# Performance work log

Hardware: AMD Instinct MI355X
Metric: run time of the kernel (lower is better)

Reference implementation:

```python
import jax, jax.numpy as jnp
import numpy as np


def setup_inputs() -> dict:
    key = jax.random.key(0)
    k1, k2 = jax.random.split(key)
    E, D, N = 1600000, 32, 100000
    e = jax.random.normal(k1, (E, D), dtype=jnp.float32)
    dst = jax.random.randint(k2, (E,), 0, N, dtype=jnp.int64)
    return {"e": e, "dst": dst, "n_nodes": N}


def reference(e, dst, n_nodes):
    # copy_e + mean reducer == segment mean of edge features over dst nodes.
    # DGL yields 0 for nodes with no in-edges.
    sums = jax.ops.segment_sum(e, dst, num_segments=n_nodes)          # [N, D]
    counts = jax.ops.segment_sum(jnp.ones((e.shape[0],), e.dtype), dst,
                                 num_segments=n_nodes)                 # [N]
    denom = jnp.maximum(counts, 1.0)[:, None]
    return sums / denom
```

## Files before the change

kernel.cpp:

```cpp
#include <hip/hip_runtime.h>
#include <hip/hip_bf16.h>


#define D_FEAT 32
#define NPB 64
#define NB_MAX 2048
#define STAGE_MAX 8192
#define CAP_MAX 2048
#define CURSOR_PAD 16

__global__ __launch_bounds__(256) void bucket_bin_kernel(
    const int* __restrict__ dst,
    int* __restrict__ cursor,
    unsigned int* __restrict__ buckets,
    int E, int nb, int cap, int chunk)
{
    __shared__ int hist[NB_MAX];
    __shared__ int offs[NB_MAX];
    __shared__ int run [NB_MAX];
    __shared__ int gpos[NB_MAX];
    __shared__ unsigned int   st_rec[STAGE_MAX];
    __shared__ unsigned short st_b  [STAGE_MAX];
    __shared__ int scan_s[256];

    int t = threadIdx.x;
    int cstart = blockIdx.x * chunk;
    int cn = E - cstart; if (cn > chunk) cn = chunk;
    if (cn <= 0) return;

    for (int i = t; i < nb; i += 256) hist[i] = 0;
    __syncthreads();

    for (int i = t; i < cn; i += 256) {
        int d = dst[cstart + i];
        atomicAdd(&hist[d >> 6], 1);
    }
    __syncthreads();

    int q = (nb + 255) / 256;
    int lo = t * q, hi = lo + q; if (hi > nb) hi = nb;
    int sum = 0;
    for (int i = lo; i < hi; i++) sum += hist[i];
    scan_s[t] = sum;
    __syncthreads();
    for (int off = 1; off < 256; off <<= 1) {
        int v = (t >= off) ? scan_s[t - off] : 0;
        __syncthreads();
        scan_s[t] += v;
        __syncthreads();
    }
    int ex = scan_s[t] - sum;
    for (int i = lo; i < hi; i++) {
        offs[i] = ex;
        run[i]  = ex;
        ex += hist[i];
    }
    __syncthreads();

    for (int i = t; i < nb; i += 256) {
        int h = hist[i];
        gpos[i] = (h > 0) ? atomicAdd(&cursor[i * CURSOR_PAD], h) : 0;
    }

    for (int i = t; i < cn; i += 256) {
        int g = cstart + i;
        int d = dst[g];
        int b = d >> 6;
        int p = atomicAdd(&run[b], 1);
        st_rec[p] = ((unsigned)g << 6) | (unsigned)(d & 63);
        st_b[p]   = (unsigned short)b;
    }
    __syncthreads();

    for (int p = t; p < cn; p += 256) {
        int b = st_b[p];
        int rel = gpos[b] + (p - offs[b]);
        if (rel < cap)
            buckets[(size_t)b * cap + rel] = st_rec[p];
    }
}

__global__ __launch_bounds__(256) void node_sort_kernel(
    const unsigned int* __restrict__ buckets,
    const int* __restrict__ cursor,
    unsigned int* __restrict__ ids2,
    int* __restrict__ startArr,
    int* __restrict__ cntArr,
    int N, int cap)
{
    __shared__ int hist[NPB];
    __shared__ int sc  [NPB];
    __shared__ int run [NPB];
    __shared__ unsigned int st[CAP_MAX];
    int t = threadIdx.x;
    int b = blockIdx.x;

    if (t < NPB) hist[t] = 0;
    __syncthreads();

    int m = cursor[b * CURSOR_PAD]; if (m > cap) m = cap;
    const unsigned int* rec = buckets + (size_t)b * cap;

    for (int i = t; i < m; i += 256)
        atomicAdd(&hist[rec[i] & 63], 1);
    __syncthreads();

    if (t < NPB) sc[t] = hist[t];
    __syncthreads();
    for (int off = 1; off < NPB; off <<= 1) {
        int v = 0;
        if (t < NPB && t >= off) v = sc[t - off];
        __syncthreads();
        if (t < NPB) sc[t] += v;
        __syncthreads();
    }
    if (t < NPB) { sc[t] -= hist[t]; run[t] = sc[t]; }
    __syncthreads();

    for (int i = t; i < m; i += 256) {
        unsigned r = rec[i];
        int p = atomicAdd(&run[r & 63], 1);
        st[p] = r >> 6;
    }
    __syncthreads();

    for (int i = t; i < m; i += 256)
        ids2[(size_t)b * cap + i] = st[i];
    if (t < NPB) {
        int node = b * NPB + t;
        if (node < N) {
            startArr[node] = b * cap + sc[t];
            cntArr[node]   = hist[t];
        }
    }
}

__global__ __launch_bounds__(256) void gather_kernel(
    const float4* __restrict__ e4,
    const unsigned int* __restrict__ ids,
    const int* __restrict__ startArr,
    const int* __restrict__ cntArr,
    float4* __restrict__ out4,
    int N, int fixed_stride)
{
    int node = blockIdx.x * 32 + (threadIdx.x >> 3);
    int j = threadIdx.x & 7;
    if (node >= N) return;
    int c = cntArr[node];
    int s;
    if (fixed_stride > 0) {
        s = node * fixed_stride;
        if (c > fixed_stride) c = fixed_stride;
    } else {
        s = startArr[node];
    }
    float4 a0 = {0.f,0.f,0.f,0.f}, a1 = {0.f,0.f,0.f,0.f};
    float4 a2 = {0.f,0.f,0.f,0.f}, a3 = {0.f,0.f,0.f,0.f};
    int k = 0;
    for (; k + 4 <= c; k += 4) {
        unsigned e0 = ids[s+k], e1 = ids[s+k+1], e2 = ids[s+k+2], e3 = ids[s+k+3];
        float4 v0 = e4[(size_t)e0*8 + j];
        float4 v1 = e4[(size_t)e1*8 + j];
        float4 v2 = e4[(size_t)e2*8 + j];
        float4 v3 = e4[(size_t)e3*8 + j];
        a0.x += v0.x; a0.y += v0.y; a0.z += v0.z; a0.w += v0.w;
        a1.x += v1.x; a1.y += v1.y; a1.z += v1.z; a1.w += v1.w;
        a2.x += v2.x; a2.y += v2.y; a2.z += v2.z; a2.w += v2.w;
        a3.x += v3.x; a3.y += v3.y; a3.z += v3.z; a3.w += v3.w;
    }
    for (; k < c; k++) {
        unsigned e0 = ids[s+k];
        float4 v0 = e4[(size_t)e0*8 + j];
        a0.x += v0.x; a0.y += v0.y; a0.z += v0.z; a0.w += v0.w;
    }
    float inv = 1.0f / (float)(c > 1 ? c : 1);
    float4 r;
    r.x = (a0.x + a1.x + a2.x + a3.x) * inv;
    r.y = (a0.y + a1.y + a2.y + a3.y) * inv;
    r.z = (a0.z + a1.z + a2.z + a3.z) * inv;
    r.w = (a0.w + a1.w + a2.w + a3.w) * inv;
    out4[(size_t)node * 8 + j] = r;
}

#define SLOT_STRIDE 64
__global__ __launch_bounds__(256) void scatter_ids_fixed(
    const int* __restrict__ dst, int* __restrict__ cursor,
    unsigned int* __restrict__ ids, int E)
{
    int i = blockIdx.x * 256 + threadIdx.x;
    if (i >= E) return;
    int d = dst[i];
    int pos = atomicAdd(&cursor[d], 1);
    if (pos < SLOT_STRIDE) ids[d * SLOT_STRIDE + pos] = (unsigned)i;
}

__global__ __launch_bounds__(256) void scatter_atomic_kernel(
    const float4* __restrict__ e4, const int* __restrict__ dst,
    float* __restrict__ sums, int* __restrict__ counts, int total)
{
    int t = blockIdx.x * 256 + threadIdx.x;
    if (t >= total) return;
    int edge = t >> 3;
    int fq = t & 7;
    float4 v = e4[t];
    int d = dst[edge];
    float* o = sums + (size_t)d * D_FEAT + fq * 4;
    atomicAdd(o + 0, v.x);
    atomicAdd(o + 1, v.y);
    atomicAdd(o + 2, v.z);
    atomicAdd(o + 3, v.w);
    if (fq == 0) atomicAdd(counts + d, 1);
}

__global__ __launch_bounds__(256) void finalize_kernel(
    float4* __restrict__ out4, const int* __restrict__ counts, int total)
{
    int t = blockIdx.x * 256 + threadIdx.x;
    if (t >= total) return;
    int node = t >> 3;
    int c = counts[node];
    float inv = 1.0f / (float)(c > 1 ? c : 1);
    float4 v = out4[t];
    v.x *= inv; v.y *= inv; v.z *= inv; v.w *= inv;
    out4[t] = v;
}

extern "C" void kernel_launch(void* const* d_in, const int* in_sizes, int n_in,
                              void* d_out, int out_size, void* d_ws, size_t ws_size,
                              hipStream_t stream) {
    const float4* e4 = (const float4*)d_in[0];
    const int* dst = (const int*)d_in[1];
    int E = in_sizes[0] / D_FEAT;
    int N = out_size / D_FEAT;

    int nb = (N + NPB - 1) / NPB;
    long long avg = (E + nb - 1) / nb;
    long long thresh = avg + 8 * (long long)(__builtin_sqrt((double)avg)) + 64;
    int cap = (int)((thresh + 63) / 64 * 64);

    char* ws = (char*)d_ws;
    size_t fast_need = (size_t)nb * CURSOR_PAD * 4
                     + (size_t)nb * cap * 4 * 2
                     + (size_t)N * 4 * 2;
    size_t r2_need = (size_t)N * 4 + (size_t)N * SLOT_STRIDE * 4;

    if (nb <= NB_MAX && cap <= CAP_MAX && ws_size >= fast_need) {
        int* cursor = (int*)ws;
        unsigned int* buckets = (unsigned int*)(ws + (size_t)nb * CURSOR_PAD * 4);
        unsigned int* ids2 = buckets + (size_t)nb * cap;
        int* startArr = (int*)(ids2 + (size_t)nb * cap);
        int* cntArr = startArr + N;

        hipMemsetAsync(cursor, 0, (size_t)nb * CURSOR_PAD * 4, stream);

        int grid1 = 256;
        int chunk = (E + grid1 - 1) / grid1;
        if (chunk > STAGE_MAX) { grid1 = (E + STAGE_MAX - 1) / STAGE_MAX; chunk = STAGE_MAX; }
        bucket_bin_kernel<<<grid1, 256, 0, stream>>>(dst, cursor, buckets, E, nb, cap, chunk);
        node_sort_kernel<<<nb, 256, 0, stream>>>(buckets, cursor, ids2, startArr, cntArr, N, cap);
        gather_kernel<<<(N + 31) / 32, 256, 0, stream>>>(e4, ids2, startArr, cntArr,
                                                         (float4*)d_out, N, 0);
    } else if (ws_size >= r2_need) {
        int* cursor = (int*)ws;
        unsigned int* ids = (unsigned int*)(ws + (size_t)N * 4);
        hipMemsetAsync(cursor, 0, (size_t)N * 4, stream);
        scatter_ids_fixed<<<(E + 255) / 256, 256, 0, stream>>>(dst, cursor, ids, E);
        gather_kernel<<<(N + 31) / 32, 256, 0, stream>>>(e4, ids, nullptr, cursor,
                                                         (float4*)d_out, N, SLOT_STRIDE);
    } else {
        int* counts = (int*)ws;
        hipMemsetAsync(d_out, 0, (size_t)out_size * sizeof(float), stream);
        hipMemsetAsync(counts, 0, (size_t)N * 4, stream);
        int total = E * (D_FEAT / 4);
        scatter_atomic_kernel<<<(total + 255) / 256, 256, 0, stream>>>(
            e4, dst, (float*)d_out, counts, total);
        int fin = N * (D_FEAT / 4);
        finalize_kernel<<<(fin + 255) / 256, 256, 0, stream>>>(
            (float4*)d_out, counts, fin);
    }
}
```

Before: 348.6 us.

## Replace two-level bucket sort with global histogram, scan and atomic scatter CSR build

Result: slower. 500.3 us (+43.5%).

```diff
diff --git a/kernel.cpp b/kernel.cpp
--- a/kernel.cpp
+++ b/kernel.cpp
@@ -1,137 +1,122 @@
 #include <hip/hip_runtime.h>
-#include <hip/hip_bf16.h>
 
 
 #define D_FEAT 32
-#define NPB 64
-#define NB_MAX 2048
-#define STAGE_MAX 8192
-#define CAP_MAX 2048
-#define CURSOR_PAD 16
-
-__global__ __launch_bounds__(256) void bucket_bin_kernel(
-    const int* __restrict__ dst,
-    int* __restrict__ cursor,
-    unsigned int* __restrict__ buckets,
-    int E, int nb, int cap, int chunk)
-{
-    __shared__ int hist[NB_MAX];
-    __shared__ int offs[NB_MAX];
-    __shared__ int run [NB_MAX];
-    __shared__ int gpos[NB_MAX];
-    __shared__ unsigned int   st_rec[STAGE_MAX];
-    __shared__ unsigned short st_b  [STAGE_MAX];
-    __shared__ int scan_s[256];
-
+#define SCAN_SPAN 1024
+
+__global__ __launch_bounds__(256) void hist_kernel(
+    const int* __restrict__ dst, int* __restrict__ cnt, int E)
+{
+    int base = (blockIdx.x * 256 + threadIdx.x) * 4;
+    if (base + 3 < E) {
+        int4 d = *(const int4*)(dst + base);
+        atomicAdd(&cnt[d.x], 1);
+        atomicAdd(&cnt[d.y], 1);
+        atomicAdd(&cnt[d.z], 1);
+        atomicAdd(&cnt[d.w], 1);
+    } else {
+        for (int i = base; i < E; i++) atomicAdd(&cnt[dst[i]], 1);
+    }
+}
+
+__global__ __launch_bounds__(256) void scan_block_sums(
+    const int* __restrict__ cnt, int* __restrict__ bsum, int N)
+{
+    __shared__ int red[256];
     int t = threadIdx.x;
-    int cstart = blockIdx.x * chunk;
-    int cn = E - cstart; if (cn > chunk) cn = chunk;
-    if (cn <= 0) return;
-
-    for (int i = t; i < nb; i += 256) hist[i] = 0;
+    int base = blockIdx.x * SCAN_SPAN + t * 4;
+    int s = 0;
+    if (base + 3 < N) {
+        int4 v = *(const int4*)(cnt + base);
+        s = v.x + v.y + v.z + v.w;
+    } else {
+        for (int i = base; i < N; i++) s += cnt[i];
+    }
+    red[t] = s;
     __syncthreads();
-
-    for (int i = t; i < cn; i += 256) {
-        int d = dst[cstart + i];
-        atomicAdd(&hist[d >> 6], 1);
-    }
-    __syncthreads();
-
-    int q = (nb + 255) / 256;
-    int lo = t * q, hi = lo + q; if (hi > nb) hi = nb;
-    int sum = 0;
-    for (int i = lo; i < hi; i++) sum += hist[i];
-    scan_s[t] = sum;
+    for (int off = 128; off > 0; off >>= 1) {
+        if (t < off) red[t] += red[t + off];
+        __syncthreads();
+    }
+    if (t == 0) bsum[blockIdx.x] = red[0];
+}
+
+__global__ __launch_bounds__(256) void scan_bases(
+    const int* __restrict__ bsum, int* __restrict__ bbase, int nblk)
+{
+    __shared__ int sc[256];
+    int t = threadIdx.x;
+    int v = (t < nblk) ? bsum[t] : 0;
+    int orig = v;
+    sc[t] = v;
     __syncthreads();
     for (int off = 1; off < 256; off <<= 1) {
-        int v = (t >= off) ? scan_s[t - off] : 0;
-        __syncthreads();
-        scan_s[t] += v;
-        __syncthreads();
-    }
-    int ex = scan_s[t] - sum;
-    for (int i = lo; i < hi; i++) {
-        offs[i] = ex;
-        run[i]  = ex;
-        ex += hist[i];
-    }
+        int u = (t >= off) ? sc[t - off] : 0;
+        __syncthreads();
+        sc[t] += u;
+        __syncthreads();
+    }
+    if (t < nblk) bbase[t] = sc[t] - orig;
+}
+
+__global__ __launch_bounds__(256) void scan_write(
+    const int* __restrict__ cnt, const int* __restrict__ bbase,
+    int* __restrict__ startArr, int* __restrict__ run, int N)
+{
+    __shared__ int sc[256];
+    int t = threadIdx.x;
+    int base = blockIdx.x * SCAN_SPAN + t * 4;
+    int c0 = 0, c1 = 0, c2 = 0, c3 = 0;
+    if (base + 3 < N) {
+        int4 v = *(const int4*)(cnt + base);
+        c0 = v.x; c1 = v.y; c2 = v.z; c3 = v.w;
+    } else {
+        if (base     < N) c0 = cnt[base];
+        if (base + 1 < N) c1 = cnt[base + 1];
+        if (base + 2 < N) c2 = cnt[base + 2];
+        if (base + 3 < N) c3 = cnt[base + 3];
+    }
+    int s = c0 + c1 + c2 + c3;
+    int orig = s;
+    sc[t] = s;
     __syncthreads();
-
-    for (int i = t; i < nb; i += 256) {
-        int h = hist[i];
-        gpos[i] = (h > 0) ? atomicAdd(&cursor[i * CURSOR_PAD], h) : 0;
-    }
-
-    for (int i = t; i < cn; i += 256) {
-        int g = cstart + i;
-        int d = dst[g];
-        int b = d >> 6;
-        int p = atomicAdd(&run[b], 1);
-        st_rec[p] = ((unsigned)g << 6) | (unsigned)(d & 63);
-        st_b[p]   = (unsigned short)b;
-    }
-    __syncthreads();
-
-    for (int p = t; p < cn; p += 256) {
-        int b = st_b[p];
-        int rel = gpos[b] + (p - offs[b]);
-        if (rel < cap)
-            buckets[(size_t)b * cap + rel] = st_rec[p];
-    }
-}
-
-__global__ __launch_bounds__(256) void node_sort_kernel(
-    const unsigned int* __restrict__ buckets,
-    const int* __restrict__ cursor,
-    unsigned int* __restrict__ ids2,
-    int* __restrict__ startArr,
-    int* __restrict__ cntArr,
-    int N, int cap)
-{
-    __shared__ int hist[NPB];
-    __shared__ int sc  [NPB];
-    __shared__ int run [NPB];
-    __shared__ unsigned int st[CAP_MAX];
-    int t = threadIdx.x;
-    int b = blockIdx.x;
-
-    if (t < NPB) hist[t] = 0;
-    __syncthreads();
-
-    int m = cursor[b * CURSOR_PAD]; if (m > cap) m = cap;
-    const unsigned int* rec = buckets + (size_t)b * cap;
-
-    for (int i = t; i < m; i += 256)
-        atomicAdd(&hist[rec[i] & 63], 1);
-    __syncthreads();
-
-    if (t < NPB) sc[t] = hist[t];
-    __syncthreads();
-    for (int off = 1; off < NPB; off <<= 1) {
-        int v = 0;
-        if (t < NPB && t >= off) v = sc[t - off];
-        __syncthreads();
-        if (t < NPB) sc[t] += v;
-        __syncthreads();
-    }
-    if (t < NPB) { sc[t] -= hist[t]; run[t] = sc[t]; }
-    __syncthreads();
-
-    for (int i = t; i < m; i += 256) {
-        unsigned r = rec[i];
-        int p = atomicAdd(&run[r & 63], 1);
-        st[p] = r >> 6;
-    }
-    __syncthreads();
-
-    for (int i = t; i < m; i += 256)
-        ids2[(size_t)b * cap + i] = st[i];
-    if (t < NPB) {
-        int node = b * NPB + t;
-        if (node < N) {
-            startArr[node] = b * cap + sc[t];
-            cntArr[node]   = hist[t];
-        }
+    for (int off = 1; off < 256; off <<= 1) {
+        int u = (t >= off) ? sc[t - off] : 0;
+        __syncthreads();
+        sc[t] += u;
+        __syncthreads();
+    }
+    int ex = bbase[blockIdx.x] + sc[t] - orig;
+    int p0 = ex, p1 = ex + c0, p2 = p1 + c1, p3 = p2 + c2;
+    if (base + 3 < N) {
+        *(int4*)(startArr + base) = make_int4(p0, p1, p2, p3);
+        *(int4*)(run + base)      = make_int4(p0, p1, p2, p3);
+    } else {
+        if (base     < N) { startArr[base]     = p0; run[base]     = p0; }
+        if (base + 1 < N) { startArr[base + 1] = p1; run[base + 1] = p1; }
+        if (base + 2 < N) { startArr[base + 2] = p2; run[base + 2] = p2; }
+        if (base + 3 < N) { startArr[base + 3] = p3; run[base + 3] = p3; }
+    }
+}
+
+__global__ __launch_bounds__(256) void scatter_kernel(
+    const int* __restrict__ dst, int* __restrict__ run,
+    unsigned int* __restrict__ ids, int E)
+{
+    int base = (blockIdx.x * 256 + threadIdx.x) * 4;
+    if (base + 3 < E) {
+        int4 d = *(const int4*)(dst + base);
+        int p0 = atomicAdd(&run[d.x], 1);
+        int p1 = atomicAdd(&run[d.y], 1);
+        int p2 = atomicAdd(&run[d.z], 1);
+        int p3 = atomicAdd(&run[d.w], 1);
+        ids[p0] = (unsigned)base;
+        ids[p1] = (unsigned)base + 1;
+        ids[p2] = (unsigned)base + 2;
+        ids[p3] = (unsigned)base + 3;
+    } else {
+        for (int i = base; i < E; i++)
+            ids[atomicAdd(&run[dst[i]], 1)] = (unsigned)i;
     }
 }
 
@@ -141,22 +126,36 @@
     const int* __restrict__ startArr,
     const int* __restrict__ cntArr,
     float4* __restrict__ out4,
-    int N, int fixed_stride)
+    int N)
 {
     int node = blockIdx.x * 32 + (threadIdx.x >> 3);
     int j = threadIdx.x & 7;
     if (node >= N) return;
     int c = cntArr[node];
-    int s;
-    if (fixed_stride > 0) {
-        s = node * fixed_stride;
-        if (c > fixed_stride) c = fixed_stride;
-    } else {
-        s = startArr[node];
-    }
+    int s = startArr[node];
     float4 a0 = {0.f,0.f,0.f,0.f}, a1 = {0.f,0.f,0.f,0.f};
     float4 a2 = {0.f,0.f,0.f,0.f}, a3 = {0.f,0.f,0.f,0.f};
     int k = 0;
+    for (; k + 8 <= c; k += 8) {
+        unsigned e0 = ids[s+k],   e1 = ids[s+k+1], e2 = ids[s+k+2], e3 = ids[s+k+3];
+        unsigned e4i = ids[s+k+4], e5 = ids[s+k+5], e6 = ids[s+k+6], e7 = ids[s+k+7];
+        float4 v0 = e4[(size_t)e0*8  + j];
+        float4 v1 = e4[(size_t)e1*8  + j];
+        float4 v2 = e4[(size_t)e2*8  + j];
+        float4 v3 = e4[(size_t)e3*8  + j];
+        float4 v4 = e4[(size_t)e4i*8 + j];
+        float4 v5 = e4[(size_t)e5*8  + j];
+        float4 v6 = e4[(size_t)e6*8  + j];
+        float4 v7 = e4[(size_t)e7*8  + j];
+        a0.x += v0.x; a0.y += v0.y; a0.z += v0.z; a0.w += v0.w;
+        a1.x += v1.x; a1.y += v1.y; a1.z += v1.z; a1.w += v1.w;
+        a2.x += v2.x; a2.y += v2.y; a2.z += v2.z; a2.w += v2.w;
+        a3.x += v3.x; a3.y += v3.y; a3.z += v3.z; a3.w += v3.w;
+        a0.x += v4.x; a0.y += v4.y; a0.z += v4.z; a0.w += v4.w;
+        a1.x += v5.x; a1.y += v5.y; a1.z += v5.z; a1.w += v5.w;
+        a2.x += v6.x; a2.y += v6.y; a2.z += v6.z; a2.w += v6.w;
+        a3.x += v7.x; a3.y += v7.y; a3.z += v7.z; a3.w += v7.w;
+    }
     for (; k + 4 <= c; k += 4) {
         unsigned e0 = ids[s+k], e1 = ids[s+k+1], e2 = ids[s+k+2], e3 = ids[s+k+3];
         float4 v0 = e4[(size_t)e0*8 + j];
@@ -180,18 +179,6 @@
     r.z = (a0.z + a1.z + a2.z + a3.z) * inv;
     r.w = (a0.w + a1.w + a2.w + a3.w) * inv;
     out4[(size_t)node * 8 + j] = r;
-}
-
-#define SLOT_STRIDE 64
-__global__ __launch_bounds__(256) void scatter_ids_fixed(
-    const int* __restrict__ dst, int* __restrict__ cursor,
-    unsigned int* __restrict__ ids, int E)
-{
-    int i = blockIdx.x * 256 + threadIdx.x;
-    if (i >= E) return;
-    int d = dst[i];
-    int pos = atomicAdd(&cursor[d], 1);
-    if (pos < SLOT_STRIDE) ids[d * SLOT_STRIDE + pos] = (unsigned)i;
 }
 
 __global__ __launch_bounds__(256) void scatter_atomic_kernel(
@@ -233,40 +220,29 @@
     int E = in_sizes[0] / D_FEAT;
     int N = out_size / D_FEAT;
 
-    int nb = (N + NPB - 1) / NPB;
-    long long avg = (E + nb - 1) / nb;
-    long long thresh = avg + 8 * (long long)(__builtin_sqrt((double)avg)) + 64;
-    int cap = (int)((thresh + 63) / 64 * 64);
+    int nblk = (N + SCAN_SPAN - 1) / SCAN_SPAN;
 
     char* ws = (char*)d_ws;
-    size_t fast_need = (size_t)nb * CURSOR_PAD * 4
-                     + (size_t)nb * cap * 4 * 2
-                     + (size_t)N * 4 * 2;
-    size_t r2_need = (size_t)N * 4 + (size_t)N * SLOT_STRIDE * 4;
-
-    if (nb <= NB_MAX && cap <= CAP_MAX && ws_size >= fast_need) {
-        int* cursor = (int*)ws;
-        unsigned int* buckets = (unsigned int*)(ws + (size_t)nb * CURSOR_PAD * 4);
-        unsigned int* ids2 = buckets + (size_t)nb * cap;
-        int* startArr = (int*)(ids2 + (size_t)nb * cap);
-        int* cntArr = startArr + N;
-
-        hipMemsetAsync(cursor, 0, (size_t)nb * CURSOR_PAD * 4, stream);
-
-        int grid1 = 256;
-        int chunk = (E + grid1 - 1) / grid1;
-        if (chunk > STAGE_MAX) { grid1 = (E + STAGE_MAX - 1) / STAGE_MAX; chunk = STAGE_MAX; }
-        bucket_bin_kernel<<<grid1, 256, 0, stream>>>(dst, cursor, buckets, E, nb, cap, chunk);
-        node_sort_kernel<<<nb, 256, 0, stream>>>(buckets, cursor, ids2, startArr, cntArr, N, cap);
-        gather_kernel<<<(N + 31) / 32, 256, 0, stream>>>(e4, ids2, startArr, cntArr,
-                                                         (float4*)d_out, N, 0);
-    } else if (ws_size >= r2_need) {
-        int* cursor = (int*)ws;
-        unsigned int* ids = (unsigned int*)(ws + (size_t)N * 4);
-        hipMemsetAsync(cursor, 0, (size_t)N * 4, stream);
-        scatter_ids_fixed<<<(E + 255) / 256, 256, 0, stream>>>(dst, cursor, ids, E);
-        gather_kernel<<<(N + 31) / 32, 256, 0, stream>>>(e4, ids, nullptr, cursor,
-                                                         (float4*)d_out, N, SLOT_STRIDE);
+    size_t need = ((size_t)3 * N + 512) * 4 + (size_t)E * 4;
+
+    if (nblk <= 256 && ws_size >= need) {
+        int* cnt      = (int*)ws;
+        int* startArr = cnt + N;
+        int* run      = startArr + N;
+        int* bsum     = run + N;
+        int* bbase    = bsum + 256;
+        unsigned int* ids = (unsigned int*)(bbase + 256);
+
+        hipMemsetAsync(cnt, 0, (size_t)N * 4, stream);
+
+        int gE = (E + 1023) / 1024;
+        hist_kernel<<<gE, 256, 0, stream>>>(dst, cnt, E);
+        scan_block_sums<<<nblk, 256, 0, stream>>>(cnt, bsum, N);
+        scan_bases<<<1, 256, 0, stream>>>(bsum, bbase, nblk);
+        scan_write<<<nblk, 256, 0, stream>>>(cnt, bbase, startArr, run, N);
+        scatter_kernel<<<gE, 256, 0, stream>>>(dst, run, ids, E);
+        gather_kernel<<<(N + 31) / 32, 256, 0, stream>>>(e4, ids, startArr, cnt,
+                                                         (float4*)d_out, N);
     } else {
         int* counts = (int*)ws;
         hipMemsetAsync(d_out, 0, (size_t)out_size * sizeof(float), stream);
```

## Fuse node sort and gather into per-bucket LDS atomic accumulation kernel

Applied to the files above, without the earlier changes.

Result: slower. 539.1 us (+54.6%).

```diff
diff --git a/kernel.cpp b/kernel.cpp
--- a/kernel.cpp
+++ b/kernel.cpp
@@ -1,28 +1,20 @@
 #include <hip/hip_runtime.h>
-#include <hip/hip_bf16.h>
 
 
 #define D_FEAT 32
 #define NPB 64
 #define NB_MAX 2048
-#define STAGE_MAX 8192
-#define CAP_MAX 2048
 #define CURSOR_PAD 16
 
-__global__ __launch_bounds__(256) void bucket_bin_kernel(
+__global__ __launch_bounds__(256) void bin_kernel(
     const int* __restrict__ dst,
     int* __restrict__ cursor,
     unsigned int* __restrict__ buckets,
     int E, int nb, int cap, int chunk)
 {
     __shared__ int hist[NB_MAX];
-    __shared__ int offs[NB_MAX];
+    __shared__ int gpos[NB_MAX];
     __shared__ int run [NB_MAX];
-    __shared__ int gpos[NB_MAX];
-    __shared__ unsigned int   st_rec[STAGE_MAX];
-    __shared__ unsigned short st_b  [STAGE_MAX];
-    __shared__ int scan_s[256];
-
     int t = threadIdx.x;
     int cstart = blockIdx.x * chunk;
     int cn = E - cstart; if (cn > chunk) cn = chunk;
@@ -31,167 +23,114 @@
     for (int i = t; i < nb; i += 256) hist[i] = 0;
     __syncthreads();
 
-    for (int i = t; i < cn; i += 256) {
-        int d = dst[cstart + i];
-        atomicAdd(&hist[d >> 6], 1);
-    }
-    __syncthreads();
-
-    int q = (nb + 255) / 256;
-    int lo = t * q, hi = lo + q; if (hi > nb) hi = nb;
-    int sum = 0;
-    for (int i = lo; i < hi; i++) sum += hist[i];
-    scan_s[t] = sum;
-    __syncthreads();
-    for (int off = 1; off < 256; off <<= 1) {
-        int v = (t >= off) ? scan_s[t - off] : 0;
-        __syncthreads();
-        scan_s[t] += v;
-        __syncthreads();
-    }
-    int ex = scan_s[t] - sum;
-    for (int i = lo; i < hi; i++) {
-        offs[i] = ex;
-        run[i]  = ex;
-        ex += hist[i];
-    }
+    int nv = cn >> 2;
+    const int4* d4 = (const int4*)(dst + cstart);
+    for (int i = t; i < nv; i += 256) {
+        int4 d = d4[i];
+        atomicAdd(&hist[d.x >> 6], 1);
+        atomicAdd(&hist[d.y >> 6], 1);
+        atomicAdd(&hist[d.z >> 6], 1);
+        atomicAdd(&hist[d.w >> 6], 1);
+    }
+    for (int i = (nv << 2) + t; i < cn; i += 256)
+        atomicAdd(&hist[dst[cstart + i] >> 6], 1);
     __syncthreads();
 
     for (int i = t; i < nb; i += 256) {
         int h = hist[i];
         gpos[i] = (h > 0) ? atomicAdd(&cursor[i * CURSOR_PAD], h) : 0;
-    }
-
-    for (int i = t; i < cn; i += 256) {
+        run[i] = 0;
+    }
+    __syncthreads();
+
+    for (int i = t; i < nv; i += 256) {
+        int4 d = d4[i];
+        int g = cstart + (i << 2);
+        int b0 = d.x >> 6, b1 = d.y >> 6, b2 = d.z >> 6, b3 = d.w >> 6;
+        int p0 = gpos[b0] + atomicAdd(&run[b0], 1);
+        int p1 = gpos[b1] + atomicAdd(&run[b1], 1);
+        int p2 = gpos[b2] + atomicAdd(&run[b2], 1);
+        int p3 = gpos[b3] + atomicAdd(&run[b3], 1);
+        if (p0 < cap) buckets[(size_t)b0 * cap + p0] = ((unsigned)(g    ) << 6) | (unsigned)(d.x & 63);
+        if (p1 < cap) buckets[(size_t)b1 * cap + p1] = ((unsigned)(g + 1) << 6) | (unsigned)(d.y & 63);
+        if (p2 < cap) buckets[(size_t)b2 * cap + p2] = ((unsigned)(g + 2) << 6) | (unsigned)(d.z & 63);
+        if (p3 < cap) buckets[(size_t)b3 * cap + p3] = ((unsigned)(g + 3) << 6) | (unsigned)(d.w & 63);
+    }
+    for (int i = (nv << 2) + t; i < cn; i += 256) {
         int g = cstart + i;
         int d = dst[g];
         int b = d >> 6;
-        int p = atomicAdd(&run[b], 1);
-        st_rec[p] = ((unsigned)g << 6) | (unsigned)(d & 63);
-        st_b[p]   = (unsigned short)b;
-    }
-    __syncthreads();
-
-    for (int p = t; p < cn; p += 256) {
-        int b = st_b[p];
-        int rel = gpos[b] + (p - offs[b]);
-        if (rel < cap)
-            buckets[(size_t)b * cap + rel] = st_rec[p];
-    }
-}
-
-__global__ __launch_bounds__(256) void node_sort_kernel(
+        int p = gpos[b] + atomicAdd(&run[b], 1);
+        if (p < cap) buckets[(size_t)b * cap + p] = ((unsigned)g << 6) | (unsigned)(d & 63);
+    }
+}
+
+__global__ __launch_bounds__(256) void bucket_accum_kernel(
+    const float4* __restrict__ e4,
     const unsigned int* __restrict__ buckets,
     const int* __restrict__ cursor,
-    unsigned int* __restrict__ ids2,
-    int* __restrict__ startArr,
-    int* __restrict__ cntArr,
+    float4* __restrict__ out4,
     int N, int cap)
 {
-    __shared__ int hist[NPB];
-    __shared__ int sc  [NPB];
-    __shared__ int run [NPB];
-    __shared__ unsigned int st[CAP_MAX];
+    __shared__ float sums[NPB][33];
+    __shared__ int cnt[NPB];
     int t = threadIdx.x;
     int b = blockIdx.x;
 
-    if (t < NPB) hist[t] = 0;
+    for (int i = t; i < NPB * 33; i += 256) ((float*)sums)[i] = 0.f;
+    if (t < NPB) cnt[t] = 0;
     __syncthreads();
 
     int m = cursor[b * CURSOR_PAD]; if (m > cap) m = cap;
     const unsigned int* rec = buckets + (size_t)b * cap;
 
-    for (int i = t; i < m; i += 256)
-        atomicAdd(&hist[rec[i] & 63], 1);
-    __syncthreads();
-
-    if (t < NPB) sc[t] = hist[t];
-    __syncthreads();
-    for (int off = 1; off < NPB; off <<= 1) {
-        int v = 0;
-        if (t < NPB && t >= off) v = sc[t - off];
-        __syncthreads();
-        if (t < NPB) sc[t] += v;
-        __syncthreads();
-    }
-    if (t < NPB) { sc[t] -= hist[t]; run[t] = sc[t]; }
-    __syncthreads();
-
-    for (int i = t; i < m; i += 256) {
-        unsigned r = rec[i];
-        int p = atomicAdd(&run[r & 63], 1);
-        st[p] = r >> 6;
-    }
-    __syncthreads();
-
-    for (int i = t; i < m; i += 256)
-        ids2[(size_t)b * cap + i] = st[i];
-    if (t < NPB) {
-        int node = b * NPB + t;
+    int g = t >> 3, j = t & 7;
+    int jb = j * 4;
+    int i = g;
+    for (; i + 96 < m; i += 128) {
+        unsigned r0 = rec[i], r1 = rec[i + 32], r2 = rec[i + 64], r3 = rec[i + 96];
+        float4 v0 = e4[(size_t)(r0 >> 6) * 8 + j];
+        float4 v1 = e4[(size_t)(r1 >> 6) * 8 + j];
+        float4 v2 = e4[(size_t)(r2 >> 6) * 8 + j];
+        float4 v3 = e4[(size_t)(r3 >> 6) * 8 + j];
+        int l0 = r0 & 63, l1 = r1 & 63, l2 = r2 & 63, l3 = r3 & 63;
+        atomicAdd(&sums[l0][jb + 0], v0.x); atomicAdd(&sums[l0][jb + 1], v0.y);
+        atomicAdd(&sums[l0][jb + 2], v0.z); atomicAdd(&sums[l0][jb + 3], v0.w);
+        atomicAdd(&sums[l1][jb + 0], v1.x); atomicAdd(&sums[l1][jb + 1], v1.y);
+        atomicAdd(&sums[l1][jb + 2], v1.z); atomicAdd(&sums[l1][jb + 3], v1.w);
+        atomicAdd(&sums[l2][jb + 0], v2.x); atomicAdd(&sums[l2][jb + 1], v2.y);
+        atomicAdd(&sums[l2][jb + 2], v2.z); atomicAdd(&sums[l2][jb + 3], v2.w);
+        atomicAdd(&sums[l3][jb + 0], v3.x); atomicAdd(&sums[l3][jb + 1], v3.y);
+        atomicAdd(&sums[l3][jb + 2], v3.z); atomicAdd(&sums[l3][jb + 3], v3.w);
+        if (j == 0) {
+            atomicAdd(&cnt[l0], 1); atomicAdd(&cnt[l1], 1);
+            atomicAdd(&cnt[l2], 1); atomicAdd(&cnt[l3], 1);
+        }
+    }
+    for (; i < m; i += 32) {
+        unsigned r0 = rec[i];
+        float4 v0 = e4[(size_t)(r0 >> 6) * 8 + j];
+        int l0 = r0 & 63;
+        atomicAdd(&sums[l0][jb + 0], v0.x); atomicAdd(&sums[l0][jb + 1], v0.y);
+        atomicAdd(&sums[l0][jb + 2], v0.z); atomicAdd(&sums[l0][jb + 3], v0.w);
+        if (j == 0) atomicAdd(&cnt[l0], 1);
+    }
+    __syncthreads();
+
+    for (int s = t; s < NPB * 8; s += 256) {
+        int local = s >> 3, jj = (s & 7) * 4;
+        int node = b * NPB + local;
         if (node < N) {
-            startArr[node] = b * cap + sc[t];
-            cntArr[node]   = hist[t];
+            int c = cnt[local];
+            float inv = 1.0f / (float)(c > 1 ? c : 1);
+            float4 r;
+            r.x = sums[local][jj + 0] * inv;
+            r.y = sums[local][jj + 1] * inv;
+            r.z = sums[local][jj + 2] * inv;
+            r.w = sums[local][jj + 3] * inv;
+            out4[(size_t)node * 8 + (s & 7)] = r;
         }
     }
-}
-
-__global__ __launch_bounds__(256) void gather_kernel(
-    const float4* __restrict__ e4,
-    const unsigned int* __restrict__ ids,
-    const int* __restrict__ startArr,
-    const int* __restrict__ cntArr,
-    float4* __restrict__ out4,
-    int N, int fixed_stride)
-{
-    int node = blockIdx.x * 32 + (threadIdx.x >> 3);
-    int j = threadIdx.x & 7;
-    if (node >= N) return;
-    int c = cntArr[node];
-    int s;
-    if (fixed_stride > 0) {
-        s = node * fixed_stride;
-        if (c > fixed_stride) c = fixed_stride;
-    } else {
-        s = startArr[node];
-    }
-    float4 a0 = {0.f,0.f,0.f,0.f}, a1 = {0.f,0.f,0.f,0.f};
-    float4 a2 = {0.f,0.f,0.f,0.f}, a3 = {0.f,0.f,0.f,0.f};
-    int k = 0;
-    for (; k + 4 <= c; k += 4) {
-        unsigned e0 = ids[s+k], e1 = ids[s+k+1], e2 = ids[s+k+2], e3 = ids[s+k+3];
-        float4 v0 = e4[(size_t)e0*8 + j];
-        float4 v1 = e4[(size_t)e1*8 + j];
-        float4 v2 = e4[(size_t)e2*8 + j];
-        float4 v3 = e4[(size_t)e3*8 + j];
-        a0.x += v0.x; a0.y += v0.y; a0.z += v0.z; a0.w += v0.w;
-        a1.x += v1.x; a1.y += v1.y; a1.z += v1.z; a1.w += v1.w;
-        a2.x += v2.x; a2.y += v2.y; a2.z += v2.z; a2.w += v2.w;
-        a3.x += v3.x; a3.y += v3.y; a3.z += v3.z; a3.w += v3.w;
-    }
-    for (; k < c; k++) {
-        unsigned e0 = ids[s+k];
-        float4 v0 = e4[(size_t)e0*8 + j];
-        a0.x += v0.x; a0.y += v0.y; a0.z += v0.z; a0.w += v0.w;
-    }
-    float inv = 1.0f / (float)(c > 1 ? c : 1);
-    float4 r;
-    r.x = (a0.x + a1.x + a2.x + a3.x) * inv;
-    r.y = (a0.y + a1.y + a2.y + a3.y) * inv;
-    r.z = (a0.z + a1.z + a2.z + a3.z) * inv;
-    r.w = (a0.w + a1.w + a2.w + a3.w) * inv;
-    out4[(size_t)node * 8 + j] = r;
-}
-
-#define SLOT_STRIDE 64
-__global__ __launch_bounds__(256) void scatter_ids_fixed(
-    const int* __restrict__ dst, int* __restrict__ cursor,
-    unsigned int* __restrict__ ids, int E)
-{
-    int i = blockIdx.x * 256 + threadIdx.x;
-    if (i >= E) return;
-    int d = dst[i];
-    int pos = atomicAdd(&cursor[d], 1);
-    if (pos < SLOT_STRIDE) ids[d * SLOT_STRIDE + pos] = (unsigned)i;
 }
 
 __global__ __launch_bounds__(256) void scatter_atomic_kernel(
@@ -240,33 +179,20 @@
 
     char* ws = (char*)d_ws;
     size_t fast_need = (size_t)nb * CURSOR_PAD * 4
-                     + (size_t)nb * cap * 4 * 2
-                     + (size_t)N * 4 * 2;
-    size_t r2_need = (size_t)N * 4 + (size_t)N * SLOT_STRIDE * 4;
-
-    if (nb <= NB_MAX && cap <= CAP_MAX && ws_size >= fast_need) {
+                     + (size_t)nb * cap * 4;
+
+    if (nb <= NB_MAX && E <= (1 << 26) && ws_size >= fast_need) {
         int* cursor = (int*)ws;
         unsigned int* buckets = (unsigned int*)(ws + (size_t)nb * CURSOR_PAD * 4);
-        unsigned int* ids2 = buckets + (size_t)nb * cap;
-        int* startArr = (int*)(ids2 + (size_t)nb * cap);
-        int* cntArr = startArr + N;
 
         hipMemsetAsync(cursor, 0, (size_t)nb * CURSOR_PAD * 4, stream);
 
-        int grid1 = 256;
-        int chunk = (E + grid1 - 1) / grid1;
-        if (chunk > STAGE_MAX) { grid1 = (E + STAGE_MAX - 1) / STAGE_MAX; chunk = STAGE_MAX; }
-        bucket_bin_kernel<<<grid1, 256, 0, stream>>>(dst, cursor, buckets, E, nb, cap, chunk);
-        node_sort_kernel<<<nb, 256, 0, stream>>>(buckets, cursor, ids2, startArr, cntArr, N, cap);
-        gather_kernel<<<(N + 31) / 32, 256, 0, stream>>>(e4, ids2, startArr, cntArr,
-                                                         (float4*)d_out, N, 0);
-    } else if (ws_size >= r2_need) {
-        int* cursor = (int*)ws;
-        unsigned int* ids = (unsigned int*)(ws + (size_t)N * 4);
-        hipMemsetAsync(cursor, 0, (size_t)N * 4, stream);
-        scatter_ids_fixed<<<(E + 255) / 256, 256, 0, stream>>>(dst, cursor, ids, E);
-        gather_kernel<<<(N + 31) / 32, 256, 0, stream>>>(e4, ids, nullptr, cursor,
-                                                         (float4*)d_out, N, SLOT_STRIDE);
+        int chunk = (E + 255) / 256;
+        chunk = (chunk + 3) & ~3;
+        int grid1 = (E + chunk - 1) / chunk;
+        bin_kernel<<<grid1, 256, 0, stream>>>(dst, cursor, buckets, E, nb, cap, chunk);
+        bucket_accum_kernel<<<nb, 256, 0, stream>>>(e4, buckets, cursor,
+                                                    (float4*)d_out, N, cap);
     } else {
         int* counts = (int*)ws;
         hipMemsetAsync(d_out, 0, (size_t)out_size * sizeof(float), stream);
```
